# Optimization experiments

Measured on AMD Instinct MI355X. Metric: run time of the kernel, lower is better.

## Reference

```python
import jax, jax.numpy as jnp
import numpy as np

B, K, SZ, D = 256, 16, 512, 8

def setup_inputs() -> dict:
    key = jax.random.key(0)
    k1, k2 = jax.random.split(key)
    x = jax.random.normal(k1, (B, SZ, D), dtype=jnp.float32)
    cluster_centers = jax.random.normal(k2, (K, SZ, D), dtype=jnp.float32)
    return {"x": x, "cluster_centers": cluster_centers}

def _dists(x, centers):
    # x: [B, sz, d]; centers: [K, sz, d]
    b, sz, d = x.shape
    k = centers.shape[0]
    # fft_sz = 2 ** int(log2(2*sz - 1) + 1)  (matches n_bits computation in normalized_cc)
    fft_sz = 2 ** int(np.log2(2 * sz - 1) + 1)
    # The module's hand-rolled dft matrix is cos(-2pi kn/N) + i sin(-2pi kn/N),
    # i.e. exactly the standard DFT of the zero-padded signal -> use jnp.fft.
    Fx = jnp.fft.fft(x, n=fft_sz, axis=1)            # [B, F, d]
    Fc = jnp.fft.fft(centers, n=fft_sz, axis=1)      # [K, F, d]
    # cc(s1, s2) = real(ifft(F1 * conj(F2))), batched over all (i, j) pairs
    prod = Fx[:, None, :, :] * jnp.conj(Fc)[None, :, :, :]   # [B, K, F, d]
    cc = jnp.real(jnp.fft.ifft(prod, axis=2))                # [B, K, F, d]
    # cc_ = cat(cc[-(sz-1):], cc[:sz])  -> length 2*sz - 1 along lag axis
    cc_cat = jnp.concatenate([cc[:, :, -(sz - 1):, :], cc[:, :, :sz, :]], axis=2)
    # norms: norm1 = Frobenius norm per sample; norm2 = arange(K) (as in forward)
    norms1 = jnp.linalg.norm(x.reshape(b, -1), axis=1)       # [B]
    norms2 = jnp.arange(k, dtype=x.dtype)                    # [K]
    denom = norms1[:, None] * norms2[None, :]                # [B, K]
    denom = jnp.where(denom < 1e-9, jnp.inf, denom)
    ncc = cc_cat.sum(axis=-1) / denom[:, :, None]            # [B, K, 2sz-1]
    return ncc.max(axis=2)                                   # [B, K]

def reference(x, cluster_centers):
    dists = _dists(x, cluster_centers)
    labels = jnp.argmin(1.0 - dists, axis=1)
    return (labels, dists)
```

## Files before the change

kernel.cpp:

```cpp
#include <hip/hip_runtime.h>
#include <math.h>


#define NB 256
#define NK 16
#define NS 512
#define ND 8
#define BAND 1120

typedef __bf16 bf16x8 __attribute__((ext_vector_type(8)));
typedef float floatx4 __attribute__((ext_vector_type(4)));

#define MFMA(q, bv, a) __builtin_amdgcn_mfma_f32_16x16x32_bf16(q, bv, a, 0, 0, 0)

__global__ __launch_bounds__(1024, 4) void kshape_kernel(
    const float* __restrict__ x, const float* __restrict__ c, float* __restrict__ out)
{
    __shared__ __align__(16) __bf16 xq[BAND * 8];
    __shared__ __align__(16) __bf16 Bf[128 * 512];
    __shared__ float wred[16][16];
    __shared__ float redn[16];
    __shared__ float s_norm;
    __shared__ float dd[16];

    const int tid = threadIdx.x;
    const int b   = blockIdx.x;

    float ss = 0.f;
    for (int jj = tid; jj < BAND; jj += 1024) {
        bf16x8 v;
        if (jj >= 511 && jj < 1023) {
            const float4* p = (const float4*)(x + ((size_t)b * NS + (size_t)(jj - 511)) * ND);
            float4 a = p[0], bb = p[1];
            ss += a.x * a.x + a.y * a.y + a.z * a.z + a.w * a.w;
            ss += bb.x * bb.x + bb.y * bb.y + bb.z * bb.z + bb.w * bb.w;
            v[0] = (__bf16)a.x;  v[1] = (__bf16)a.y;  v[2] = (__bf16)a.z;  v[3] = (__bf16)a.w;
            v[4] = (__bf16)bb.x; v[5] = (__bf16)bb.y; v[6] = (__bf16)bb.z; v[7] = (__bf16)bb.w;
        } else {
            #pragma unroll
            for (int e = 0; e < 8; ++e) v[e] = (__bf16)0.0f;
        }
        *(bf16x8*)(xq + (size_t)jj * 8) = v;
    }

    #pragma unroll 4
    for (int i = 0; i < 8; ++i) {
        int idx = tid + i * 1024;
        int kc = idx >> 6, Lf = idx & 63;
        int n = Lf & 15, qd = Lf >> 4;
        const float4* src = (const float4*)(c + ((size_t)n * NS + (size_t)(kc * 4 + qd)) * ND);
        float4 a = src[0], bb = src[1];
        bf16x8 v;
        v[0] = (__bf16)a.x;  v[1] = (__bf16)a.y;  v[2] = (__bf16)a.z;  v[3] = (__bf16)a.w;
        v[4] = (__bf16)bb.x; v[5] = (__bf16)bb.y; v[6] = (__bf16)bb.z; v[7] = (__bf16)bb.w;
        *(bf16x8*)(Bf + (size_t)idx * 8) = v;
    }

    #pragma unroll
    for (int off = 32; off; off >>= 1) ss += __shfl_down(ss, off);
    if ((tid & 63) == 0) redn[tid >> 6] = ss;
    __syncthreads();
    if (tid == 0) {
        float t = 0.f;
        #pragma unroll
        for (int i = 0; i < 16; ++i) t += redn[i];
        s_norm = sqrtf(t);
    }

    const int L    = tid & 63;
    const int m    = L & 15;
    const int quad = L >> 4;
    const int wu   = __builtin_amdgcn_readfirstlane(tid >> 6);

    const int a0  = 112 - 16 * wu;
    const int klo = (a0 > 0) ? a0 : 0;
    const int kh_ = (1022 - 64 * wu) >> 2;
    const int khi = (kh_ > 127) ? 127 : kh_;

    const __bf16* gb = xq + 8 * (64 * wu + m + quad);
    const __bf16* Bl = Bf + L * 8;

    bf16x8 Q[16];
    #pragma unroll
    for (int i = 0; i < 16; ++i) Q[i] = *(const bf16x8*)(gb + 32 * (klo + i));

    bf16x8 Bv[4];
    #pragma unroll
    for (int i = 0; i < 4; ++i) Bv[i] = *(const bf16x8*)(Bl + (size_t)(klo + i) * 512);

    floatx4 acc[4] = {};

    for (int kc0 = klo; kc0 <= khi; kc0 += 16) {
        #pragma unroll
        for (int s = 0; s < 16; ++s) {
            const int kc = kc0 + s;
            bf16x8 bcur = Bv[s & 3];
            acc[0] = MFMA(Q[(s + 0)  & 15], bcur, acc[0]);
            acc[1] = MFMA(Q[(s + 4)  & 15], bcur, acc[1]);
            acc[2] = MFMA(Q[(s + 8)  & 15], bcur, acc[2]);
            acc[3] = MFMA(Q[(s + 12) & 15], bcur, acc[3]);
            Q[s & 15] = *(const bf16x8*)(gb + 32 * (kc + 16));
            Bv[s & 3] = *(const bf16x8*)(Bl + (size_t)((kc + 4) & 127) * 512);
        }
    }

    float vmax = -INFINITY;
    #pragma unroll
    for (int r = 0; r < 4; ++r) {
        #pragma unroll
        for (int e = 0; e < 4; ++e) {
            bool phantom = (wu == 15) & (r == 3) & (quad == 3) & (e == 3);
            vmax = fmaxf(vmax, phantom ? -INFINITY : acc[r][e]);
        }
    }
    vmax = fmaxf(vmax, __shfl_xor(vmax, 16));
    vmax = fmaxf(vmax, __shfl_xor(vmax, 32));
    if (quad == 0) wred[wu][m] = vmax;
    __syncthreads();

    if (tid < 16) {
        float mm = wred[0][tid];
        #pragma unroll
        for (int i = 1; i < 16; ++i) mm = fmaxf(mm, wred[i][tid]);
        float denom = s_norm * (float)tid;
        float d = (denom < 1e-9f) ? 0.f : mm / denom;
        dd[tid] = d;
        out[NB + b * NK + tid] = d;
    }
    __syncthreads();
    if (tid == 0) {
        float best = dd[0]; int lab = 0;
        #pragma unroll
        for (int k = 1; k < NK; ++k) if (dd[k] > best) { best = dd[k]; lab = k; }
        out[b] = (float)lab;
    }
}

extern "C" void kernel_launch(void* const* d_in, const int* in_sizes, int n_in,
                              void* d_out, int out_size, void* d_ws, size_t ws_size,
                              hipStream_t stream) {
    const float* x = (const float*)d_in[0];
    const float* c = (const float*)d_in[1];
    float* out = (float*)d_out;
    kshape_kernel<<<NB, 1024, 0, stream>>>(x, c, out);
}
```

Measured before the change: 74.09 us.

## Split x padding/norm into prep kernel and read padded x from global memory

Adds a separate prep kernel that converts x to a zero-padded bf16 buffer in workspace and computes per-sample norms. The main kernel then streams its Q operands straight from global memory (through cache) instead of staging them in LDS, which frees LDS and removes one synchronization stage. The B tile is extended with zero rows so the wrap-around mask is no longer needed. The cost is an extra kernel launch and a global round-trip for the padded x, and the MFMA loop's loads now carry global rather than LDS latency.

```diff
diff --git a/kernel.cpp b/kernel.cpp
--- a/kernel.cpp
+++ b/kernel.cpp
@@ -6,28 +6,23 @@
 #define NK 16
 #define NS 512
 #define ND 8
-#define BAND 1120
+#define XROWS 1120
 
 typedef __bf16 bf16x8 __attribute__((ext_vector_type(8)));
 typedef float floatx4 __attribute__((ext_vector_type(4)));
 
 #define MFMA(q, bv, a) __builtin_amdgcn_mfma_f32_16x16x32_bf16(q, bv, a, 0, 0, 0)
 
-__global__ __launch_bounds__(1024, 4) void kshape_kernel(
-    const float* __restrict__ x, const float* __restrict__ c, float* __restrict__ out)
+__global__ __launch_bounds__(256) void prep_kernel(
+    const float* __restrict__ x, __bf16* __restrict__ xpad, float* __restrict__ wsfn)
 {
-    __shared__ __align__(16) __bf16 xq[BAND * 8];
-    __shared__ __align__(16) __bf16 Bf[128 * 512];
-    __shared__ float wred[16][16];
-    __shared__ float redn[16];
-    __shared__ float s_norm;
-    __shared__ float dd[16];
-
+    __shared__ float redn[4];
     const int tid = threadIdx.x;
     const int b   = blockIdx.x;
+    __bf16* dst = xpad + (size_t)b * XROWS * 8;
 
     float ss = 0.f;
-    for (int jj = tid; jj < BAND; jj += 1024) {
+    for (int jj = tid; jj < XROWS; jj += 256) {
         bf16x8 v;
         if (jj >= 511 && jj < 1023) {
             const float4* p = (const float4*)(x + ((size_t)b * NS + (size_t)(jj - 511)) * ND);
@@ -40,8 +35,25 @@
             #pragma unroll
             for (int e = 0; e < 8; ++e) v[e] = (__bf16)0.0f;
         }
-        *(bf16x8*)(xq + (size_t)jj * 8) = v;
+        *(bf16x8*)(dst + (size_t)jj * 8) = v;
     }
+    #pragma unroll
+    for (int off = 32; off; off >>= 1) ss += __shfl_down(ss, off);
+    if ((tid & 63) == 0) redn[tid >> 6] = ss;
+    __syncthreads();
+    if (tid == 0) wsfn[b] = sqrtf(redn[0] + redn[1] + redn[2] + redn[3]);
+}
+
+__global__ __launch_bounds__(1024, 4) void kshape_kernel(
+    const __bf16* __restrict__ xpad, const float* __restrict__ c,
+    const float* __restrict__ wsfn, float* __restrict__ out)
+{
+    __shared__ __align__(16) __bf16 Bf[132 * 512];
+    __shared__ float wred[16][16];
+    __shared__ float dd[16];
+
+    const int tid = threadIdx.x;
+    const int b   = blockIdx.x;
 
     #pragma unroll 4
     for (int i = 0; i < 8; ++i) {
@@ -55,17 +67,13 @@
         v[4] = (__bf16)bb.x; v[5] = (__bf16)bb.y; v[6] = (__bf16)bb.z; v[7] = (__bf16)bb.w;
         *(bf16x8*)(Bf + (size_t)idx * 8) = v;
     }
-
-    #pragma unroll
-    for (int off = 32; off; off >>= 1) ss += __shfl_down(ss, off);
-    if ((tid & 63) == 0) redn[tid >> 6] = ss;
+    if (tid < 256) {
+        bf16x8 z;
+        #pragma unroll
+        for (int e = 0; e < 8; ++e) z[e] = (__bf16)0.0f;
+        *(bf16x8*)(Bf + (size_t)(8192 + tid) * 8) = z;
+    }
     __syncthreads();
-    if (tid == 0) {
-        float t = 0.f;
-        #pragma unroll
-        for (int i = 0; i < 16; ++i) t += redn[i];
-        s_norm = sqrtf(t);
-    }
 
     const int L    = tid & 63;
     const int m    = L & 15;
@@ -77,12 +85,12 @@
     const int kh_ = (1022 - 64 * wu) >> 2;
     const int khi = (kh_ > 127) ? 127 : kh_;
 
-    const __bf16* gb = xq + 8 * (64 * wu + m + quad);
+    const __bf16* ga = xpad + (size_t)b * XROWS * 8 + 8 * (64 * wu + m + quad);
     const __bf16* Bl = Bf + L * 8;
 
     bf16x8 Q[16];
     #pragma unroll
-    for (int i = 0; i < 16; ++i) Q[i] = *(const bf16x8*)(gb + 32 * (klo + i));
+    for (int i = 0; i < 16; ++i) Q[i] = *(const bf16x8*)(ga + 32 * (klo + i));
 
     bf16x8 Bv[4];
     #pragma unroll
@@ -99,8 +107,8 @@
             acc[1] = MFMA(Q[(s + 4)  & 15], bcur, acc[1]);
             acc[2] = MFMA(Q[(s + 8)  & 15], bcur, acc[2]);
             acc[3] = MFMA(Q[(s + 12) & 15], bcur, acc[3]);
-            Q[s & 15] = *(const bf16x8*)(gb + 32 * (kc + 16));
-            Bv[s & 3] = *(const bf16x8*)(Bl + (size_t)((kc + 4) & 127) * 512);
+            Q[s & 15] = *(const bf16x8*)(ga + 32 * (kc + 16));
+            Bv[s & 3] = *(const bf16x8*)(Bl + (size_t)(kc + 4) * 512);
         }
     }
 
@@ -122,7 +130,7 @@
         float mm = wred[0][tid];
         #pragma unroll
         for (int i = 1; i < 16; ++i) mm = fmaxf(mm, wred[i][tid]);
-        float denom = s_norm * (float)tid;
+        float denom = wsfn[b] * (float)tid;
         float d = (denom < 1e-9f) ? 0.f : mm / denom;
         dd[tid] = d;
         out[NB + b * NK + tid] = d;
@@ -141,6 +149,10 @@
                               hipStream_t stream) {
     const float* x = (const float*)d_in[0];
     const float* c = (const float*)d_in[1];
-    float* out = (float*)d_out;
-    kshape_kernel<<<NB, 1024, 0, stream>>>(x, c, out);
+    float* out  = (float*)d_out;
+    float* wsfn = (float*)d_ws;
+    __bf16* xpad = (__bf16*)((char*)d_ws + 4096);
+
+    prep_kernel<<<NB, 256, 0, stream>>>(x, xpad, wsfn);
+    kshape_kernel<<<NB, 1024, 0, stream>>>(xpad, c, wsfn, out);
 }
```

Result: slower. 78.62 us (+6.1%).

## Quantize inputs to int8 and use i8 MFMA for cross-correlation

Applied to the files above, without the earlier changes.

Replaces the bf16 MFMA correlation with int8 MFMA (16x16x64), quantizing x per-batch and each center per-cluster using absmax scaling, then rescaling the integer max back to float. The LDS layout becomes even/odd-shifted int8 copies of x so K=64 chunks align with lags. This halves LDS footprint and doubles MFMA throughput per instruction. It adds an absmax reduction pass and loses precision, which may change argmax labels or exceed tolerance.

```diff
diff --git a/kernel.cpp b/kernel.cpp
--- a/kernel.cpp
+++ b/kernel.cpp
@@ -6,124 +6,158 @@
 #define NK 16
 #define NS 512
 #define ND 8
-#define BAND 1120
 
-typedef __bf16 bf16x8 __attribute__((ext_vector_type(8)));
-typedef float floatx4 __attribute__((ext_vector_type(4)));
+typedef int intx4 __attribute__((ext_vector_type(4)));
 
-#define MFMA(q, bv, a) __builtin_amdgcn_mfma_f32_16x16x32_bf16(q, bv, a, 0, 0, 0)
+#define MFMA_I8(a, b, c) __builtin_amdgcn_mfma_i32_16x16x64_i8(a, b, c, 0, 0, 0)
+
+__device__ __forceinline__ int q8(float v, float s) {
+    return (int)rintf(fminf(fmaxf(v * s, -127.f), 127.f));
+}
+__device__ __forceinline__ unsigned pk4(int a, int b, int c, int d) {
+    return (a & 255) | ((b & 255) << 8) | ((c & 255) << 16) | ((unsigned)(d & 255) << 24);
+}
 
 __global__ __launch_bounds__(1024, 4) void kshape_kernel(
     const float* __restrict__ x, const float* __restrict__ c, float* __restrict__ out)
 {
-    __shared__ __align__(16) __bf16 xq[BAND * 8];
-    __shared__ __align__(16) __bf16 Bf[128 * 512];
-    __shared__ float wred[16][16];
-    __shared__ float redn[16];
-    __shared__ float s_norm;
+    __shared__ __align__(16) char xqE[560 * 16];
+    __shared__ __align__(16) char xqO[560 * 16];
+    __shared__ __align__(16) char Bq[68 * 64 * 16];
+    __shared__ float Mc[16];
+    __shared__ float redn[16], redm[16];
+    __shared__ float s_Mb, s_nrm;
+    __shared__ int   wredi[16][16];
     __shared__ float dd[16];
 
     const int tid = threadIdx.x;
     const int b   = blockIdx.x;
+    const int L   = tid & 63;
+    const int wu  = __builtin_amdgcn_readfirstlane(tid >> 6);
 
-    float ss = 0.f;
-    for (int jj = tid; jj < BAND; jj += 1024) {
-        bf16x8 v;
-        if (jj >= 511 && jj < 1023) {
-            const float4* p = (const float4*)(x + ((size_t)b * NS + (size_t)(jj - 511)) * ND);
-            float4 a = p[0], bb = p[1];
-            ss += a.x * a.x + a.y * a.y + a.z * a.z + a.w * a.w;
-            ss += bb.x * bb.x + bb.y * bb.y + bb.z * bb.z + bb.w * bb.w;
-            v[0] = (__bf16)a.x;  v[1] = (__bf16)a.y;  v[2] = (__bf16)a.z;  v[3] = (__bf16)a.w;
-            v[4] = (__bf16)bb.x; v[5] = (__bf16)bb.y; v[6] = (__bf16)bb.z; v[7] = (__bf16)bb.w;
-        } else {
-            #pragma unroll
-            for (int e = 0; e < 8; ++e) v[e] = (__bf16)0.0f;
-        }
-        *(bf16x8*)(xq + (size_t)jj * 8) = v;
+    {
+        int4 z = {0, 0, 0, 0};
+        if (tid < 560) { ((int4*)xqE)[tid] = z; ((int4*)xqO)[tid] = z; }
+        if (tid < 256) ((int4*)(Bq + 64 * 64 * 16))[tid] = z;
     }
 
-    #pragma unroll 4
-    for (int i = 0; i < 8; ++i) {
-        int idx = tid + i * 1024;
-        int kc = idx >> 6, Lf = idx & 63;
-        int n = Lf & 15, qd = Lf >> 4;
-        const float4* src = (const float4*)(c + ((size_t)n * NS + (size_t)(kc * 4 + qd)) * ND);
-        float4 a = src[0], bb = src[1];
-        bf16x8 v;
-        v[0] = (__bf16)a.x;  v[1] = (__bf16)a.y;  v[2] = (__bf16)a.z;  v[3] = (__bf16)a.w;
-        v[4] = (__bf16)bb.x; v[5] = (__bf16)bb.y; v[6] = (__bf16)bb.z; v[7] = (__bf16)bb.w;
-        *(bf16x8*)(Bf + (size_t)idx * 8) = v;
+    const float4* x4 = (const float4*)(x + (size_t)b * (NS * ND));
+    float4 v = x4[tid];
+    float am = fmaxf(fmaxf(fabsf(v.x), fabsf(v.y)), fmaxf(fabsf(v.z), fabsf(v.w)));
+    float ss = v.x * v.x + v.y * v.y + v.z * v.z + v.w * v.w;
+    const float4* cw = (const float4*)(c + (size_t)wu * (NS * ND));
+    float cm = 0.f;
+    #pragma unroll
+    for (int i = 0; i < 16; ++i) {
+        float4 w = cw[L + 64 * i];
+        cm = fmaxf(cm, fmaxf(fmaxf(fabsf(w.x), fabsf(w.y)), fmaxf(fabsf(w.z), fabsf(w.w))));
     }
+    #pragma unroll
+    for (int off = 32; off; off >>= 1) {
+        ss += __shfl_down(ss, off);
+        am = fmaxf(am, __shfl_down(am, off));
+        cm = fmaxf(cm, __shfl_down(cm, off));
+    }
+    if (L == 0) { redn[wu] = ss; redm[wu] = am; Mc[wu] = cm; }
+    __syncthreads();
 
+    float Mb = redm[0];
     #pragma unroll
-    for (int off = 32; off; off >>= 1) ss += __shfl_down(ss, off);
-    if ((tid & 63) == 0) redn[tid >> 6] = ss;
-    __syncthreads();
+    for (int i = 1; i < 16; ++i) Mb = fmaxf(Mb, redm[i]);
     if (tid == 0) {
         float t = 0.f;
         #pragma unroll
         for (int i = 0; i < 16; ++i) t += redn[i];
-        s_norm = sqrtf(t);
+        s_nrm = sqrtf(t);
+        s_Mb  = Mb;
     }
 
-    const int L    = tid & 63;
+    const float sx = (Mb > 0.f) ? 127.f / Mb : 0.f;
+    if (tid < 512) {
+        int row = 511 + tid;
+        float4 a = x4[2 * tid], bb = x4[2 * tid + 1];
+        unsigned lo = pk4(q8(a.x, sx), q8(a.y, sx), q8(a.z, sx), q8(a.w, sx));
+        unsigned hi = pk4(q8(bb.x, sx), q8(bb.y, sx), q8(bb.z, sx), q8(bb.w, sx));
+        uint2 pr = make_uint2(lo, hi);
+        *(uint2*)(xqE + (row >> 1) * 16 + (row & 1) * 8) = pr;
+        int lineO = (row & 1) ? (row >> 1) : (row >> 1) - 1;
+        int offO  = (row & 1) ? 0 : 8;
+        *(uint2*)(xqO + lineO * 16 + offO) = pr;
+    }
+
+    #pragma unroll
+    for (int i = 0; i < 4; ++i) {
+        int f = tid + 1024 * i;
+        int kc = f >> 6, Lf = f & 63, n = Lf & 15, qd = Lf >> 4;
+        int t0 = 8 * kc + 2 * qd;
+        const float4* cn = (const float4*)(c + (size_t)n * (NS * ND));
+        float4 a = cn[2 * t0], b2 = cn[2 * t0 + 1], c2 = cn[2 * t0 + 2], d2 = cn[2 * t0 + 3];
+        float sc = (Mc[n] > 0.f) ? 127.f / Mc[n] : 0.f;
+        int4 w;
+        w.x = pk4(q8(a.x, sc), q8(a.y, sc), q8(a.z, sc), q8(a.w, sc));
+        w.y = pk4(q8(b2.x, sc), q8(b2.y, sc), q8(b2.z, sc), q8(b2.w, sc));
+        w.z = pk4(q8(c2.x, sc), q8(c2.y, sc), q8(c2.z, sc), q8(c2.w, sc));
+        w.w = pk4(q8(d2.x, sc), q8(d2.y, sc), q8(d2.z, sc), q8(d2.w, sc));
+        ((int4*)Bq)[f] = w;
+    }
+    __syncthreads();
+
     const int m    = L & 15;
     const int quad = L >> 4;
-    const int wu   = __builtin_amdgcn_readfirstlane(tid >> 6);
+    const int a0  = 56 - 8 * wu;
+    const int klo = (a0 > 0) ? a0 : 0;
+    const int kh_ = 127 - 8 * wu;
+    const int khi = (kh_ > 63) ? 63 : kh_;
 
-    const int a0  = 112 - 16 * wu;
-    const int klo = (a0 > 0) ? a0 : 0;
-    const int kh_ = (1022 - 64 * wu) >> 2;
-    const int khi = (kh_ > 127) ? 127 : kh_;
+    const char* base = ((m & 1) == 0) ? xqE : xqO;
+    const char* ga   = base + ((((64 * wu + m) - (m & 1)) >> 1) + quad) * 16;
+    const char* Bl = Bq + L * 16;
 
-    const __bf16* gb = xq + 8 * (64 * wu + m + quad);
-    const __bf16* Bl = Bf + L * 8;
+    intx4 Q[8];
+    #pragma unroll
+    for (int i = 0; i < 8; ++i) Q[i] = *(const intx4*)(ga + 64 * (klo + i));
+    intx4 Bv[4];
+    #pragma unroll
+    for (int i = 0; i < 4; ++i) Bv[i] = *(const intx4*)(Bl + (size_t)(klo + i) * 1024);
 
-    bf16x8 Q[16];
-    #pragma unroll
-    for (int i = 0; i < 16; ++i) Q[i] = *(const bf16x8*)(gb + 32 * (klo + i));
+    intx4 acc[4] = {};
 
-    bf16x8 Bv[4];
-    #pragma unroll
-    for (int i = 0; i < 4; ++i) Bv[i] = *(const bf16x8*)(Bl + (size_t)(klo + i) * 512);
-
-    floatx4 acc[4] = {};
-
-    for (int kc0 = klo; kc0 <= khi; kc0 += 16) {
+    for (int kc0 = klo; kc0 <= khi; kc0 += 8) {
         #pragma unroll
-        for (int s = 0; s < 16; ++s) {
+        for (int s = 0; s < 8; ++s) {
             const int kc = kc0 + s;
-            bf16x8 bcur = Bv[s & 3];
-            acc[0] = MFMA(Q[(s + 0)  & 15], bcur, acc[0]);
-            acc[1] = MFMA(Q[(s + 4)  & 15], bcur, acc[1]);
-            acc[2] = MFMA(Q[(s + 8)  & 15], bcur, acc[2]);
-            acc[3] = MFMA(Q[(s + 12) & 15], bcur, acc[3]);
-            Q[s & 15] = *(const bf16x8*)(gb + 32 * (kc + 16));
-            Bv[s & 3] = *(const bf16x8*)(Bl + (size_t)((kc + 4) & 127) * 512);
+            intx4 bcur = Bv[s & 3];
+            acc[0] = MFMA_I8(Q[(s + 0) & 7], bcur, acc[0]);
+            acc[1] = MFMA_I8(Q[(s + 2) & 7], bcur, acc[1]);
+            acc[2] = MFMA_I8(Q[(s + 4) & 7], bcur, acc[2]);
+            acc[3] = MFMA_I8(Q[(s + 6) & 7], bcur, acc[3]);
+            Q[s & 7]  = *(const intx4*)(ga + 64 * (kc + 8));
+            Bv[s & 3] = *(const intx4*)(Bl + (size_t)(kc + 4) * 1024);
         }
     }
 
-    float vmax = -INFINITY;
+    int vmax = (int)0x80000000;
     #pragma unroll
     for (int r = 0; r < 4; ++r) {
         #pragma unroll
         for (int e = 0; e < 4; ++e) {
             bool phantom = (wu == 15) & (r == 3) & (quad == 3) & (e == 3);
-            vmax = fmaxf(vmax, phantom ? -INFINITY : acc[r][e]);
+            int val = phantom ? (int)0x80000000 : acc[r][e];
+            vmax = (val > vmax) ? val : vmax;
         }
     }
-    vmax = fmaxf(vmax, __shfl_xor(vmax, 16));
-    vmax = fmaxf(vmax, __shfl_xor(vmax, 32));
-    if (quad == 0) wred[wu][m] = vmax;
+    { int o = __shfl_xor(vmax, 16); vmax = (o > vmax) ? o : vmax; }
+    { int o = __shfl_xor(vmax, 32); vmax = (o > vmax) ? o : vmax; }
+    if (quad == 0) wredi[wu][m] = vmax;
     __syncthreads();
 
     if (tid < 16) {
-        float mm = wred[0][tid];
+        int mm = wredi[0][tid];
         #pragma unroll
-        for (int i = 1; i < 16; ++i) mm = fmaxf(mm, wred[i][tid]);
-        float denom = s_norm * (float)tid;
-        float d = (denom < 1e-9f) ? 0.f : mm / denom;
+        for (int i = 1; i < 16; ++i) mm = (wredi[i][tid] > mm) ? wredi[i][tid] : mm;
+        float scale = s_Mb * Mc[tid] * (1.0f / 16129.0f);
+        float denom = s_nrm * (float)tid;
+        float d = (denom < 1e-9f) ? 0.f : ((float)mm * scale) / denom;
         dd[tid] = d;
         out[NB + b * NK + tid] = d;
     }
```

Result: faster. 70.63 us (-4.7%).
